# Kernel optimization log

Hardware: AMD Instinct MI355X
Metric: run time of the kernel (lower is better)

Reference implementation:

```python
import jax, jax.numpy as jnp
import numpy as np

B, KEY, D, U, MODES = 16384, 64, 128, 128, 32

def setup_inputs() -> dict:
    key = jax.random.key(0)
    k1, k2, k3, k4, k5 = jax.random.split(key, 5)
    return {
        "key": jax.random.normal(k1, (B, KEY), dtype=jnp.float32),
        "x": jax.random.normal(k2, (B, D), dtype=jnp.float32),
        "sens": jnp.ones((MODES,), dtype=jnp.float32),
        "keys_map": jax.random.normal(k3, (MODES, KEY), dtype=jnp.float32),
        "kernels": jax.random.normal(k4, (MODES, D, U), dtype=jnp.float32) * 0.05,
        "biases": jax.random.normal(k5, (MODES, U), dtype=jnp.float32) * 0.05,
    }

def reference(key, x, sens, keys_map, kernels, biases):
    # key: [B, KEY]; keys_map: [MODES, KEY]
    # Euclidean distance of each key to each mode's stored key.
    dist = jnp.sqrt(jnp.sum((key[:, None, :] - keys_map[None, :, :]) ** 2, axis=-1))  # [B, MODES]
    sim = jax.nn.softmax(sens / (dist + 1.0), axis=-1)  # [B, MODES]
    modes = kernels.shape[0]
    # Original: kernel_b = mean_m(sim[b,m] * kernels[m]); out_b = x_b @ kernel_b.
    # Reordered as GEMM-per-mode + weighted combine (same math):
    out = jnp.einsum('bm,bd,mdu->bu', sim, x, kernels) / modes  # [B, U]
    out = out + (sim @ biases) / modes  # mean over modes of sim-weighted biases
    return out
```

## Files before the change

kernel.cpp:

```cpp
#include <hip/hip_runtime.h>

#define BATCH 16384
#define KEYD  64
#define DDIM  128
#define UDIM  128
#define MODES 32

typedef __attribute__((ext_vector_type(8))) short bf16x8;
typedef __attribute__((ext_vector_type(4))) float f32x4;

__device__ __forceinline__ unsigned short f2bf(float f) {
  unsigned u = __float_as_uint(f);
  unsigned r = (u + 0x7FFFu + ((u >> 16) & 1u)) >> 16;
  return (unsigned short)r;
}

__device__ __forceinline__ void gld_lds16(const void* g, void* l) {
  __builtin_amdgcn_global_load_lds(
      (const __attribute__((address_space(1))) unsigned int*)g,
      (__attribute__((address_space(3))) unsigned int*)l, 16, 0, 0);
}

__global__ __launch_bounds__(256) void prep_all(
    const float* __restrict__ key, const float* __restrict__ x,
    const float* __restrict__ sens, const float* __restrict__ keys_map,
    const float* __restrict__ kernels, const float* __restrict__ biases,
    float* __restrict__ sim, float* __restrict__ simT,
    unsigned short* __restrict__ x16,
    unsigned short* __restrict__ kb16, unsigned short* __restrict__ bb16) {
  const int t = threadIdx.x;
  const int bid = blockIdx.x;

  if (bid < BATCH / 32) {
    __shared__ float kr[32][KEYD];
    __shared__ float sims[32][33];
    *(float4*)(&kr[0][0] + t * 4) =
        *(const float4*)(key + (long)bid * 32 * KEYD + t * 4);
    *(float4*)(&kr[0][0] + 1024 + t * 4) =
        *(const float4*)(key + (long)bid * 32 * KEYD + 1024 + t * 4);

    const int lane = t & 63, wave = t >> 6;
    const int m = lane & 31, h = lane >> 5;
    float kreg[32];
    {
      const float* kmp = keys_map + m * KEYD + h * 32;
      #pragma unroll
      for (int j = 0; j < 32; j += 4) {
        const float4 v = *(const float4*)(kmp + j);
        kreg[j] = v.x; kreg[j + 1] = v.y; kreg[j + 2] = v.z; kreg[j + 3] = v.w;
      }
    }
    const float sv = sens[m];
    __syncthreads();

    #pragma unroll
    for (int rr = 0; rr < 8; ++rr) {
      const int rl = wave * 8 + rr;
      const long row = (long)bid * 32 + rl;

      float d2h = 0.f;
      #pragma unroll
      for (int j = 0; j < 32; j += 2) {
        const float2 kv = *(const float2*)(&kr[rl][h * 32 + j]);
        float a = kv.x - kreg[j], b = kv.y - kreg[j + 1];
        d2h += a * a + b * b;
      }
      float d2 = d2h + __shfl_xor(d2h, 32, 64);
      float logit = sv / (sqrtf(d2) + 1.0f);
      float mx = logit;
      #pragma unroll
      for (int off = 16; off > 0; off >>= 1) mx = fmaxf(mx, __shfl_xor(mx, off, 64));
      float e = __expf(logit - mx);
      float s = e;
      #pragma unroll
      for (int off = 16; off > 0; off >>= 1) s += __shfl_xor(s, off, 64);
      if (h == 0) {
        const float p = e / s;
        sim[row * MODES + m] = p;
        sims[m][rl] = p;
      }

      const float2 xv = *(const float2*)(x + row * DDIM + lane * 2);
      ushort2 o; o.x = f2bf(xv.x); o.y = f2bf(xv.y);
      *(ushort2*)(x16 + row * DDIM + lane * 2) = o;
    }

    __syncthreads();
    {
      const int m2 = t >> 3, r0 = (t & 7) * 4;
      float4 v;
      v.x = sims[m2][r0 + 0]; v.y = sims[m2][r0 + 1];
      v.z = sims[m2][r0 + 2]; v.w = sims[m2][r0 + 3];
      *(float4*)(simT + (long)m2 * BATCH + (long)bid * 32 + r0) = v;
    }
  } else {
    int tt = (bid - BATCH / 32) * 256 + t;
    if (tt < MODES * 16 * UDIM) {
      int u = tt & 127, kb = (tt >> 7) & 15, m = tt >> 11;
      const float* src = kernels + (long)((m * 16 + kb) * 8) * UDIM + u;
      ushort4 lo, hi;
      lo.x = f2bf(src[0 * UDIM]); lo.y = f2bf(src[1 * UDIM]);
      lo.z = f2bf(src[2 * UDIM]); lo.w = f2bf(src[3 * UDIM]);
      hi.x = f2bf(src[4 * UDIM]); hi.y = f2bf(src[5 * UDIM]);
      hi.z = f2bf(src[6 * UDIM]); hi.w = f2bf(src[7 * UDIM]);
      *(ushort4*)(kb16 + (long)tt * 8) = lo;
      *(ushort4*)(kb16 + (long)tt * 8 + 4) = hi;
    } else {
      int tb = tt - MODES * 16 * UDIM;
      int u = tb & 127, kb = tb >> 7;
      const float* src = biases + kb * 8 * UDIM + u;
      ushort4 lo, hi;
      lo.x = f2bf(src[0 * UDIM]); lo.y = f2bf(src[1 * UDIM]);
      lo.z = f2bf(src[2 * UDIM]); lo.w = f2bf(src[3 * UDIM]);
      hi.x = f2bf(src[4 * UDIM]); hi.y = f2bf(src[5 * UDIM]);
      hi.z = f2bf(src[6 * UDIM]); hi.w = f2bf(src[7 * UDIM]);
      *(ushort4*)(bb16 + (long)tb * 8) = lo;
      *(ushort4*)(bb16 + (long)tb * 8 + 4) = hi;
    }
  }
}

__global__ __launch_bounds__(512, 2) void gemm_strip(
    const unsigned short* __restrict__ x16, const unsigned short* __restrict__ kb16,
    const unsigned short* __restrict__ bb16, const float* __restrict__ sim,
    const float* __restrict__ simT, float* __restrict__ out) {
  __shared__ alignas(16) unsigned short bshB[256 * 16 * 8];

  const int t = threadIdx.x;
  const int lane = t & 63, w = t >> 6;
  const int q = lane >> 4, l16 = lane & 15;
  const int bid = blockIdx.x;
  const int group = bid & 31, strip = bid >> 5;
  const long bm = (long)group * 512;
  const int wrow = w * 64;

  #pragma unroll
  for (int i = 0; i < 8; ++i) {
    const int j = i * 8 + w;
    const int c = 4 * j + (lane >> 4);
    const int m_l = c >> 4, kb = c & 15;
    gld_lds16(kb16 + ((long)m_l * 16 + kb) * (UDIM * 8) + (strip * 16 + (lane & 15)) * 8,
              &bshB[(c * 16 + (lane & 15)) * 8]);
  }

  bf16x8 aF[4][4];
  #pragma unroll
  for (int rt = 0; rt < 4; ++rt)
    #pragma unroll
    for (int ks = 0; ks < 4; ++ks)
      aF[rt][ks] = *(const bf16x8*)(x16 + (bm + wrow + rt * 16 + l16) * DDIM + ks * 32 + q * 8);

  __syncthreads();

  bf16x8 pf[8];
  #pragma unroll
  for (int i = 0; i < 8; ++i) {
    const int j = i * 8 + w;
    const int c = 4 * j + (lane >> 4);
    const int m_l = c >> 4, kb = c & 15;
    pf[i] = *(const bf16x8*)(kb16 + ((long)(16 + m_l) * 16 + kb) * (UDIM * 8)
                             + (strip * 16 + (lane & 15)) * 8);
  }

  f32x4 acc[4] = {};
  const float* svbase = simT + bm + wrow + q * 4;

#define LOAD_SV(dst, mg)                                                        \
  { _Pragma("unroll")                                                           \
    for (int rt = 0; rt < 4; ++rt)                                              \
      dst[rt] = *(const f32x4*)(svbase + (long)(mg) * BATCH + rt * 16); }

#define COMPUTE_MODE(ml, SV)                                                    \
  { bf16x8 bF[4];                                                               \
    _Pragma("unroll")                                                           \
    for (int ks = 0; ks < 4; ++ks)                                              \
      bF[ks] = *(const bf16x8*)&bshB[(((ml) * 16 + ks * 4 + q) * 16 + l16) * 8];\
    _Pragma("unroll")                                                           \
    for (int rt = 0; rt < 4; ++rt) {                                            \
      f32x4 t0 = {}, t1 = {};                                                   \
      t0 = __builtin_amdgcn_mfma_f32_16x16x32_bf16(aF[rt][0], bF[0], t0, 0, 0, 0); \
      t1 = __builtin_amdgcn_mfma_f32_16x16x32_bf16(aF[rt][1], bF[1], t1, 0, 0, 0); \
      t0 = __builtin_amdgcn_mfma_f32_16x16x32_bf16(aF[rt][2], bF[2], t0, 0, 0, 0); \
      t1 = __builtin_amdgcn_mfma_f32_16x16x32_bf16(aF[rt][3], bF[3], t1, 0, 0, 0); \
      acc[rt] += SV[rt] * (t0 + t1);                                            \
    } }

  for (int h = 0; h < 2; ++h) {
    if (h == 1) {
      __syncthreads();
      #pragma unroll
      for (int i = 0; i < 8; ++i) {
        const int j = i * 8 + w;
        const int c = 4 * j + (lane >> 4);
        *(bf16x8*)&bshB[(c * 16 + (lane & 15)) * 8] = pf[i];
      }
      __syncthreads();
    }
    f32x4 svA[4], svB[4];
    LOAD_SV(svA, h * 16);
    #pragma unroll 2
    for (int ml = 0; ml < 16; ml += 2) {
      LOAD_SV(svB, h * 16 + ml + 1);
      COMPUTE_MODE(ml, svA);
      if (ml + 2 < 16) LOAD_SV(svA, h * 16 + ml + 2);
      COMPUTE_MODE(ml + 1, svB);
    }
  }
#undef LOAD_SV
#undef COMPUTE_MODE

  {
    const bf16x8 bb = *(const bf16x8*)(bb16 + ((long)q * UDIM + strip * 16 + l16) * 8);
    #pragma unroll
    for (int rt = 0; rt < 4; ++rt) {
      const float* sp = sim + (bm + wrow + rt * 16 + l16) * MODES + q * 8;
      const float4 sv0 = *(const float4*)(sp);
      const float4 sv1 = *(const float4*)(sp + 4);
      bf16x8 sF;
      sF[0] = (short)f2bf(sv0.x); sF[1] = (short)f2bf(sv0.y);
      sF[2] = (short)f2bf(sv0.z); sF[3] = (short)f2bf(sv0.w);
      sF[4] = (short)f2bf(sv1.x); sF[5] = (short)f2bf(sv1.y);
      sF[6] = (short)f2bf(sv1.z); sF[7] = (short)f2bf(sv1.w);
      acc[rt] = __builtin_amdgcn_mfma_f32_16x16x32_bf16(sF, bb, acc[rt], 0, 0, 0);
    }
  }

  #pragma unroll
  for (int rt = 0; rt < 4; ++rt) {
    const long row = bm + wrow + rt * 16 + q * 4;
    #pragma unroll
    for (int r = 0; r < 4; ++r)
      out[(row + r) * UDIM + strip * 16 + l16] = acc[rt][r] * (1.0f / MODES);
  }
}

extern "C" void kernel_launch(void* const* d_in, const int* in_sizes, int n_in,
                              void* d_out, int out_size, void* d_ws, size_t ws_size,
                              hipStream_t stream) {
  const float* key      = (const float*)d_in[0];
  const float* x        = (const float*)d_in[1];
  const float* sens     = (const float*)d_in[2];
  const float* keys_map = (const float*)d_in[3];
  const float* kernels  = (const float*)d_in[4];
  const float* biases   = (const float*)d_in[5];
  float* out = (float*)d_out;

  char* ws = (char*)d_ws;
  float*          sim  = (float*)ws;
  unsigned short* x16  = (unsigned short*)(ws + (2u << 20));
  unsigned short* kb16 = (unsigned short*)(ws + (6u << 20));
  unsigned short* bb16 = (unsigned short*)(ws + (7u << 20));
  float*          simT = (float*)(ws + (8u << 20));

  prep_all<<<BATCH / 32 + 258, 256, 0, stream>>>(
      key, x, sens, keys_map, kernels, biases, sim, simT, x16, kb16, bb16);
  gemm_strip<<<dim3(256), 512, 0, stream>>>(x16, kb16, bb16, sim, simT, out);
}
```

Baseline: 115.6 us.

## Convert x to bf16 inside GEMM kernel and prefetch B fragments from LDS

Drops the separate bf16 copy of x written by the prep kernel. The GEMM kernel now loads fp32 x directly and converts it in registers, which removes a 4MB write and 4MB read through the workspace. It also double-buffers the B fragments read from LDS across the mode loop and fully unrolls that loop so LDS reads overlap the MFMAs. The cost is more register pressure under the (512,2) launch bounds, and each strip block now reads twice as many bytes of x.

After: 106.0 us (median of 2 runs). 1.09x faster.

```diff
diff --git a/kernel.cpp b/kernel.cpp
--- a/kernel.cpp
+++ b/kernel.cpp
@@ -22,11 +22,10 @@
 }
 
 __global__ __launch_bounds__(256) void prep_all(
-    const float* __restrict__ key, const float* __restrict__ x,
-    const float* __restrict__ sens, const float* __restrict__ keys_map,
-    const float* __restrict__ kernels, const float* __restrict__ biases,
+    const float* __restrict__ key, const float* __restrict__ sens,
+    const float* __restrict__ keys_map, const float* __restrict__ kernels,
+    const float* __restrict__ biases,
     float* __restrict__ sim, float* __restrict__ simT,
-    unsigned short* __restrict__ x16,
     unsigned short* __restrict__ kb16, unsigned short* __restrict__ bb16) {
   const int t = threadIdx.x;
   const int bid = blockIdx.x;
@@ -79,10 +78,6 @@
         sim[row * MODES + m] = p;
         sims[m][rl] = p;
       }
-
-      const float2 xv = *(const float2*)(x + row * DDIM + lane * 2);
-      ushort2 o; o.x = f2bf(xv.x); o.y = f2bf(xv.y);
-      *(ushort2*)(x16 + row * DDIM + lane * 2) = o;
     }
 
     __syncthreads();
@@ -121,7 +116,7 @@
 }
 
 __global__ __launch_bounds__(512, 2) void gemm_strip(
-    const unsigned short* __restrict__ x16, const unsigned short* __restrict__ kb16,
+    const float* __restrict__ x, const unsigned short* __restrict__ kb16,
     const unsigned short* __restrict__ bb16, const float* __restrict__ sim,
     const float* __restrict__ simT, float* __restrict__ out) {
   __shared__ alignas(16) unsigned short bshB[256 * 16 * 8];
@@ -147,8 +142,17 @@
   #pragma unroll
   for (int rt = 0; rt < 4; ++rt)
     #pragma unroll
-    for (int ks = 0; ks < 4; ++ks)
-      aF[rt][ks] = *(const bf16x8*)(x16 + (bm + wrow + rt * 16 + l16) * DDIM + ks * 32 + q * 8);
+    for (int ks = 0; ks < 4; ++ks) {
+      const float* xp = x + (bm + wrow + rt * 16 + l16) * DDIM + ks * 32 + q * 8;
+      const float4 a0 = *(const float4*)(xp);
+      const float4 a1 = *(const float4*)(xp + 4);
+      bf16x8 f;
+      f[0] = (short)f2bf(a0.x); f[1] = (short)f2bf(a0.y);
+      f[2] = (short)f2bf(a0.z); f[3] = (short)f2bf(a0.w);
+      f[4] = (short)f2bf(a1.x); f[5] = (short)f2bf(a1.y);
+      f[6] = (short)f2bf(a1.z); f[7] = (short)f2bf(a1.w);
+      aF[rt][ks] = f;
+    }
 
   __syncthreads();
 
@@ -170,18 +174,19 @@
     for (int rt = 0; rt < 4; ++rt)                                              \
       dst[rt] = *(const f32x4*)(svbase + (long)(mg) * BATCH + rt * 16); }
 
-#define COMPUTE_MODE(ml, SV)                                                    \
-  { bf16x8 bF[4];                                                               \
-    _Pragma("unroll")                                                           \
+#define LOAD_BF(dst, ml)                                                        \
+  { _Pragma("unroll")                                                           \
     for (int ks = 0; ks < 4; ++ks)                                              \
-      bF[ks] = *(const bf16x8*)&bshB[(((ml) * 16 + ks * 4 + q) * 16 + l16) * 8];\
-    _Pragma("unroll")                                                           \
+      dst[ks] = *(const bf16x8*)&bshB[(((ml) * 16 + ks * 4 + q) * 16 + l16) * 8]; }
+
+#define COMPUTE_MODE(BF, SV)                                                    \
+  { _Pragma("unroll")                                                           \
     for (int rt = 0; rt < 4; ++rt) {                                            \
       f32x4 t0 = {}, t1 = {};                                                   \
-      t0 = __builtin_amdgcn_mfma_f32_16x16x32_bf16(aF[rt][0], bF[0], t0, 0, 0, 0); \
-      t1 = __builtin_amdgcn_mfma_f32_16x16x32_bf16(aF[rt][1], bF[1], t1, 0, 0, 0); \
-      t0 = __builtin_amdgcn_mfma_f32_16x16x32_bf16(aF[rt][2], bF[2], t0, 0, 0, 0); \
-      t1 = __builtin_amdgcn_mfma_f32_16x16x32_bf16(aF[rt][3], bF[3], t1, 0, 0, 0); \
+      t0 = __builtin_amdgcn_mfma_f32_16x16x32_bf16(aF[rt][0], BF[0], t0, 0, 0, 0); \
+      t1 = __builtin_amdgcn_mfma_f32_16x16x32_bf16(aF[rt][1], BF[1], t1, 0, 0, 0); \
+      t0 = __builtin_amdgcn_mfma_f32_16x16x32_bf16(aF[rt][2], BF[2], t0, 0, 0, 0); \
+      t1 = __builtin_amdgcn_mfma_f32_16x16x32_bf16(aF[rt][3], BF[3], t1, 0, 0, 0); \
       acc[rt] += SV[rt] * (t0 + t1);                                            \
     } }
 
@@ -197,16 +202,23 @@
       __syncthreads();
     }
     f32x4 svA[4], svB[4];
+    bf16x8 bFA[4], bFB[4];
     LOAD_SV(svA, h * 16);
-    #pragma unroll 2
+    LOAD_BF(bFA, 0);
+    #pragma unroll
     for (int ml = 0; ml < 16; ml += 2) {
       LOAD_SV(svB, h * 16 + ml + 1);
-      COMPUTE_MODE(ml, svA);
-      if (ml + 2 < 16) LOAD_SV(svA, h * 16 + ml + 2);
-      COMPUTE_MODE(ml + 1, svB);
+      LOAD_BF(bFB, ml + 1);
+      COMPUTE_MODE(bFA, svA);
+      if (ml + 2 < 16) {
+        LOAD_SV(svA, h * 16 + ml + 2);
+        LOAD_BF(bFA, ml + 2);
+      }
+      COMPUTE_MODE(bFB, svB);
     }
   }
 #undef LOAD_SV
+#undef LOAD_BF
 #undef COMPUTE_MODE
 
   {
@@ -247,12 +259,11 @@
 
   char* ws = (char*)d_ws;
   float*          sim  = (float*)ws;
-  unsigned short* x16  = (unsigned short*)(ws + (2u << 20));
-  unsigned short* kb16 = (unsigned short*)(ws + (6u << 20));
-  unsigned short* bb16 = (unsigned short*)(ws + (7u << 20));
-  float*          simT = (float*)(ws + (8u << 20));
+  float*          simT = (float*)(ws + (2u << 20));
+  unsigned short* kb16 = (unsigned short*)(ws + (4u << 20));
+  unsigned short* bb16 = (unsigned short*)(ws + (5u << 20));
 
   prep_all<<<BATCH / 32 + 258, 256, 0, stream>>>(
-      key, x, sens, keys_map, kernels, biases, sim, simT, x16, kb16, bb16);
-  gemm_strip<<<dim3(256), 512, 0, stream>>>(x16, kb16, bb16, sim, simT, out);
-}
+      key, sens, keys_map, kernels, biases, sim, simT, kb16, bb16);
+  gemm_strip<<<dim3(256), 512, 0, stream>>>(x, kb16, bb16, sim, simT, out);
+}
```
